# Kernel optimization log

Hardware: AMD Instinct MI355X
Metric: run time of the kernel (lower is better)

Reference implementation:

```python
import jax, jax.numpy as jnp
import numpy as np

N_NODES = 170000
N_EDGES = 1200000
IN_FEATS = 128
N_HIDDEN = 256
N_CLASSES = 40
BN_EPS = 1e-5


def setup_inputs() -> dict:
    key = jax.random.key(0)
    ks = jax.random.split(key, 12)
    feat = jax.random.normal(ks[0], (N_NODES, IN_FEATS), dtype=jnp.float32)
    src = jax.random.randint(ks[1], (N_EDGES,), 0, N_NODES, dtype=jnp.int32)
    dst = jax.random.randint(ks[2], (N_EDGES,), 0, N_NODES, dtype=jnp.int32)
    # GraphConv weights (glorot-ish scale) and last-layer bias
    W0 = jax.random.normal(ks[3], (IN_FEATS, N_HIDDEN), dtype=jnp.float32) * (1.0 / np.sqrt(IN_FEATS))
    W1 = jax.random.normal(ks[4], (N_HIDDEN, N_HIDDEN), dtype=jnp.float32) * (1.0 / np.sqrt(N_HIDDEN))
    W2 = jax.random.normal(ks[5], (N_HIDDEN, N_CLASSES), dtype=jnp.float32) * (1.0 / np.sqrt(N_HIDDEN))
    b2 = jnp.zeros((N_CLASSES,), dtype=jnp.float32)
    # BatchNorm affine params for the two hidden layers
    g0 = jnp.ones((N_HIDDEN,), dtype=jnp.float32)
    beta0 = jnp.zeros((N_HIDDEN,), dtype=jnp.float32)
    g1 = jnp.ones((N_HIDDEN,), dtype=jnp.float32)
    beta1 = jnp.zeros((N_HIDDEN,), dtype=jnp.float32)
    return {"feat": feat, "src": src, "dst": dst, "W0": W0, "W1": W1, "W2": W2,
            "b2": b2, "g0": g0, "beta0": beta0, "g1": g1, "beta1": beta1}


def _batchnorm(h, gamma, beta):
    mean = jnp.mean(h, axis=0)
    var = jnp.mean((h - mean) ** 2, axis=0)  # biased var, torch training-mode norm
    return (h - mean) * jax.lax.rsqrt(var + BN_EPS) * gamma + beta


def reference(feat, src, dst, W0, W1, W2, b2, g0, beta0, g1, beta1):
    n = feat.shape[0]
    ones_e = jnp.ones(src.shape, dtype=feat.dtype)
    deg_out = jnp.clip(jax.ops.segment_sum(ones_e, src, num_segments=n), 1.0)
    deg_in = jnp.clip(jax.ops.segment_sum(ones_e, dst, num_segments=n), 1.0)
    norm_src = deg_out ** -0.5  # [N]
    norm_dst = deg_in ** -0.5   # [N]

    def conv(h, W, bias=None):
        # GraphConv 'both': D_out^{-1/2} message, sum-aggregate, D_in^{-1/2}
        h = h @ W                              # project first (out <= in)
        msg = h[src] * norm_src[src][:, None]  # [E, out]
        agg = jax.ops.segment_sum(msg, dst, num_segments=n) * norm_dst[:, None]
        if bias is not None:
            agg = agg + bias
        return agg

    # dropout layers are identity in this deterministic (eval-style) reference
    h = conv(feat, W0)
    h = jax.nn.relu(_batchnorm(h, g0, beta0))
    h = conv(h, W1)
    h = jax.nn.relu(_batchnorm(h, g1, beta1))
    h = conv(h, W2, b2)
    return h
```

## Files before the change

### kernel.cpp

```cpp
#include <hip/hip_runtime.h>

#define NN 170000
#define NE 1200000
#define F_IN 128
#define F_HID 256
#define F_OUT 40
#define BN_EPS 1e-5f
#define SCAN_B ((NN + 255) / 256)

typedef __attribute__((ext_vector_type(8))) short short8;
typedef __attribute__((ext_vector_type(4))) float f32x4;
typedef __attribute__((ext_vector_type(4))) unsigned short us4;

__device__ __forceinline__ float b2f(unsigned short u) {
    union { unsigned x; float f; } c; c.x = ((unsigned)u) << 16; return c.f;
}
__device__ __forceinline__ unsigned short f2b(float f) {
    union { float f; unsigned x; } c; c.f = f;
    unsigned r = (c.x + 0x7FFFu + ((c.x >> 16) & 1u)) >> 16;
    return (unsigned short)r;
}
__device__ __forceinline__ unsigned bn2(unsigned u, float a0, float b0, float a1, float b1) {
    float lo = b2f((unsigned short)(u & 0xffffu));
    float hi = b2f((unsigned short)(u >> 16));
    lo = fmaxf(lo * a0 + b0, 0.0f);
    hi = fmaxf(hi * a1 + b1, 0.0f);
    return (unsigned)f2b(lo) | ((unsigned)f2b(hi) << 16);
}

__global__ void count_kernel(const int* __restrict__ src, const int* __restrict__ dst,
                             int* __restrict__ cnt_src, int* __restrict__ cnt_dst, int E) {
    int e = blockIdx.x * blockDim.x + threadIdx.x;
    if (e < E) {
        atomicAdd(&cnt_src[src[e]], 1);
        atomicAdd(&cnt_dst[dst[e]], 1);
    }
}

__global__ void norm_kernel(const int* __restrict__ cnt_src, const int* __restrict__ cnt_dst,
                            float* __restrict__ norm_src, float* __restrict__ norm_dst, int N) {
    int i = blockIdx.x * blockDim.x + threadIdx.x;
    if (i < N) {
        norm_src[i] = rsqrtf((float)max(cnt_src[i], 1));
        norm_dst[i] = rsqrtf((float)max(cnt_dst[i], 1));
    }
}

__global__ void scan_block_kernel(const int* __restrict__ cnt, int* __restrict__ local,
                                  int* __restrict__ partials, int N) {
    __shared__ int s[256];
    int t = threadIdx.x;
    int idx = blockIdx.x * 256 + t;
    int v = (idx < N) ? cnt[idx] : 0;
    s[t] = v;
    __syncthreads();
    #pragma unroll
    for (int off = 1; off < 256; off <<= 1) {
        int x = (t >= off) ? s[t - off] : 0;
        __syncthreads();
        s[t] += x;
        __syncthreads();
    }
    if (idx < N) local[idx] = s[t] - v;
    if (t == 255) partials[blockIdx.x] = s[t];
}

__global__ void scan_partials_kernel(int* __restrict__ partials, int B) {
    __shared__ int s[1024];
    int t = threadIdx.x;
    int v = (t < B) ? partials[t] : 0;
    s[t] = v;
    __syncthreads();
    #pragma unroll
    for (int off = 1; off < 1024; off <<= 1) {
        int x = (t >= off) ? s[t - off] : 0;
        __syncthreads();
        s[t] += x;
        __syncthreads();
    }
    if (t < B) partials[t] = s[t] - v;
}

__global__ void scan_add_kernel(const int* __restrict__ local, const int* __restrict__ partials,
                                int* __restrict__ row_ptr, int N) {
    int idx = blockIdx.x * blockDim.x + threadIdx.x;
    if (idx < N) row_ptr[idx] = local[idx] + partials[idx >> 8];
    if (idx == 0) row_ptr[N] = NE;
}

__global__ void fill_kernel(const int* __restrict__ src, const int* __restrict__ dst,
                            const int* __restrict__ row_ptr, int* __restrict__ fill,
                            int* __restrict__ csr_src, int E) {
    int e = blockIdx.x * blockDim.x + threadIdx.x;
    if (e < E) {
        int d = dst[e];
        int pos = row_ptr[d] + atomicAdd(&fill[d], 1);
        csr_src[pos] = src[e];
    }
}

__global__ void cast_feat_kernel(const float* __restrict__ feat, unsigned short* __restrict__ featb) {
    unsigned idx = blockIdx.x * blockDim.x + threadIdx.x;
    if (idx >= (unsigned)NN * (F_IN / 4)) return;
    const float* p = feat + (size_t)idx * 4;
    f32x4 v = __builtin_nontemporal_load((const f32x4*)p);
    us4 o; o.x = f2b(v.x); o.y = f2b(v.y); o.z = f2b(v.z); o.w = f2b(v.w);
    *(us4*)(featb + (size_t)idx * 4) = o;
}

__global__ void gather0_kernel(const unsigned short* __restrict__ h, const int* __restrict__ row_ptr,
                               const int* __restrict__ csr_src, const float* __restrict__ norm_src,
                               unsigned short* __restrict__ out, int N) {
    constexpr int TPN = F_IN / 4;
    unsigned idx = blockIdx.x * blockDim.x + threadIdx.x;
    if (idx >= (unsigned)N * TPN) return;
    unsigned node = idx / TPN;
    unsigned g = idx % TPN;
    int beg = row_ptr[node], end = row_ptr[node + 1];
    float ax = 0.f, ay = 0.f, az = 0.f, aw = 0.f;
    for (int e = beg; e < end; e++) {
        int s = csr_src[e];
        float ns = norm_src[s];
        const us4 v = *(const us4*)(h + (size_t)s * F_IN + g * 4);
        ax += b2f(v.x) * ns; ay += b2f(v.y) * ns; az += b2f(v.z) * ns; aw += b2f(v.w) * ns;
    }
    us4 o; o.x = f2b(ax); o.y = f2b(ay); o.z = f2b(az); o.w = f2b(aw);
    __builtin_nontemporal_store(o, (us4*)(out + (size_t)node * F_IN + g * 4));
}

__global__ void gather1_bn_kernel(const unsigned short* __restrict__ h, const int* __restrict__ row_ptr,
                                  const int* __restrict__ csr_src, const float* __restrict__ norm_src,
                                  const float* __restrict__ bna, const float* __restrict__ bnb,
                                  unsigned short* __restrict__ out, int N) {
    constexpr int TPN = F_HID / 4;
    unsigned idx = blockIdx.x * blockDim.x + threadIdx.x;
    if (idx >= (unsigned)N * TPN) return;
    unsigned node = idx / TPN;
    unsigned g = idx % TPN;
    const f32x4 a4 = *(const f32x4*)(bna + g * 4);
    const f32x4 b4 = *(const f32x4*)(bnb + g * 4);
    int beg = row_ptr[node], end = row_ptr[node + 1];
    float ax = 0.f, ay = 0.f, az = 0.f, aw = 0.f;
    for (int e = beg; e < end; e++) {
        int s = csr_src[e];
        float ns = norm_src[s];
        const us4 v = *(const us4*)(h + (size_t)s * F_HID + g * 4);
        ax += fmaxf(b2f(v.x) * a4.x + b4.x, 0.f) * ns;
        ay += fmaxf(b2f(v.y) * a4.y + b4.y, 0.f) * ns;
        az += fmaxf(b2f(v.z) * a4.z + b4.z, 0.f) * ns;
        aw += fmaxf(b2f(v.w) * a4.w + b4.w, 0.f) * ns;
    }
    us4 o; o.x = f2b(ax); o.y = f2b(ay); o.z = f2b(az); o.w = f2b(aw);
    __builtin_nontemporal_store(o, (us4*)(out + (size_t)node * F_HID + g * 4));
}

__global__ void gather_final_kernel(const float* __restrict__ h, const int* __restrict__ row_ptr,
                                    const int* __restrict__ csr_src, const float* __restrict__ norm_src,
                                    const float* __restrict__ norm_dst, const float* __restrict__ bias,
                                    float* __restrict__ out, int N) {
    constexpr int TPN = F_OUT / 4;
    unsigned idx = blockIdx.x * blockDim.x + threadIdx.x;
    if (idx >= (unsigned)N * TPN) return;
    unsigned node = idx / TPN;
    unsigned g = idx % TPN;
    int beg = row_ptr[node], end = row_ptr[node + 1];
    float ax = 0.f, ay = 0.f, az = 0.f, aw = 0.f;
    for (int e = beg; e < end; e++) {
        int s = csr_src[e];
        float ns = norm_src[s];
        const f32x4 v = *(const f32x4*)(h + (size_t)s * F_OUT + g * 4);
        ax += v.x * ns; ay += v.y * ns; az += v.z * ns; aw += v.w * ns;
    }
    float nd = norm_dst[node];
    const f32x4 b = *(const f32x4*)(bias + g * 4);
    f32x4 r;
    r.x = ax * nd + b.x; r.y = ay * nd + b.y; r.z = az * nd + b.z; r.w = aw * nd + b.w;
    __builtin_nontemporal_store(r, (f32x4*)(out + (size_t)node * F_OUT + g * 4));
}

template<int K, int M, int MP>
__global__ void wt_kernel(const float* __restrict__ W, unsigned short* __restrict__ Wt) {
    int idx = blockIdx.x * blockDim.x + threadIdx.x;
    if (idx >= MP * K) return;
    int m = idx / K, k = idx % K;
    float v = (m < M) ? W[(size_t)k * M + m] : 0.0f;
    Wt[idx] = f2b(v);
}

__global__ void bn_finalize_kernel(const float* __restrict__ sum, const float* __restrict__ sumsq,
                                   const float* __restrict__ gamma, const float* __restrict__ beta,
                                   float* __restrict__ a, float* __restrict__ b) {
    int c = threadIdx.x;
    float invN = 1.0f / (float)NN;
    float mean = sum[c] * invN;
    float var = sumsq[c] * invN - mean * mean;
    float inv = rsqrtf(var + BN_EPS);
    float ac = inv * gamma[c];
    a[c] = ac;
    b[c] = beta[c] - mean * ac;
}

template<int K, int BN_T, int WM_T, int WN_T, int WAVES_N, bool SCALE, bool BF16OUT, int M_OUT,
         bool STATS, bool APPLYBN>
__global__ __launch_bounds__(256) void mfma_gemm(const unsigned short* __restrict__ A,
                                                 const unsigned short* __restrict__ Wt,
                                                 const float* __restrict__ norm_dst,
                                                 void* __restrict__ C,
                                                 const float* __restrict__ bna,
                                                 const float* __restrict__ bnb,
                                                 float* __restrict__ osum,
                                                 float* __restrict__ osumsq, int N) {
    constexpr int BM = 128, BK = 64, AP = 72;
    __shared__ unsigned short As[BM * AP];
    __shared__ unsigned short Bs[BN_T * AP];

    const int lane = threadIdx.x & 63;
    const int wave = threadIdx.x >> 6;
    const int wr = wave / WAVES_N, wc = wave % WAVES_N;
    const int quad = lane >> 4, l15 = lane & 15;
    const int r0 = blockIdx.y * BM;
    const int c0 = blockIdx.x * BN_T;
    const int wmb = wr * WM_T * 16;
    const int wnb = wc * WN_T * 16;

    f32x4 acc[WM_T][WN_T] = {};

    for (int k0 = 0; k0 < K; k0 += BK) {
        #pragma unroll
        for (int p = 0; p < BM * (BK / 8) / 256; p++) {
            int c = threadIdx.x + p * 256;
            int row = c >> 3, off = (c & 7) * 8;
            int gr = r0 + row;
            uint4 v = make_uint4(0, 0, 0, 0);
            if (gr < N) {
                v = *(const uint4*)(A + (size_t)gr * K + k0 + off);
                if (APPLYBN) {
                    int kb = k0 + off;
                    const f32x4 a0 = *(const f32x4*)(bna + kb);
                    const f32x4 a1 = *(const f32x4*)(bna + kb + 4);
                    const f32x4 s0 = *(const f32x4*)(bnb + kb);
                    const f32x4 s1 = *(const f32x4*)(bnb + kb + 4);
                    v.x = bn2(v.x, a0.x, s0.x, a0.y, s0.y);
                    v.y = bn2(v.y, a0.z, s0.z, a0.w, s0.w);
                    v.z = bn2(v.z, a1.x, s1.x, a1.y, s1.y);
                    v.w = bn2(v.w, a1.z, s1.z, a1.w, s1.w);
                }
            }
            *(uint4*)(As + row * AP + off) = v;
        }
        #pragma unroll
        for (int p = 0; p < BN_T * (BK / 8) / 256; p++) {
            int c = threadIdx.x + p * 256;
            int m = c >> 3, off = (c & 7) * 8;
            *(uint4*)(Bs + m * AP + off) = *(const uint4*)(Wt + (size_t)(c0 + m) * K + k0 + off);
        }
        __syncthreads();
        #pragma unroll
        for (int kk = 0; kk < BK; kk += 32) {
            short8 af[WM_T], bf[WN_T];
            #pragma unroll
            for (int i = 0; i < WM_T; i++)
                af[i] = *(const short8*)(As + (wmb + i * 16 + l15) * AP + kk + quad * 8);
            #pragma unroll
            for (int j = 0; j < WN_T; j++)
                bf[j] = *(const short8*)(Bs + (wnb + j * 16 + l15) * AP + kk + quad * 8);
            #pragma unroll
            for (int i = 0; i < WM_T; i++)
                #pragma unroll
                for (int j = 0; j < WN_T; j++)
                    acc[i][j] = __builtin_amdgcn_mfma_f32_16x16x32_bf16(af[i], bf[j], acc[i][j], 0, 0, 0);
        }
        __syncthreads();
    }

    float s[WN_T] = {}, ss[WN_T] = {};
    #pragma unroll
    for (int i = 0; i < WM_T; i++) {
        #pragma unroll
        for (int r = 0; r < 4; r++) {
            int row = r0 + wmb + i * 16 + quad * 4 + r;
            if (row >= N) continue;
            float scale = SCALE ? norm_dst[row] : 1.0f;
            #pragma unroll
            for (int j = 0; j < WN_T; j++) {
                float v = acc[i][j][r] * scale;
                if (STATS) { s[j] += v; ss[j] += v * v; }
                int col = c0 + wnb + j * 16 + l15;
                if (col < M_OUT) {
                    if (BF16OUT) ((unsigned short*)C)[(size_t)row * M_OUT + col] = f2b(v);
                    else         ((float*)C)[(size_t)row * M_OUT + col] = v;
                }
            }
        }
    }
    if (STATS) {
        #pragma unroll
        for (int j = 0; j < WN_T; j++) {
            float t = s[j], t2 = ss[j];
            t  += __shfl_xor(t, 16);  t  += __shfl_xor(t, 32);
            t2 += __shfl_xor(t2, 16); t2 += __shfl_xor(t2, 32);
            if (quad == 0) {
                int col = c0 + wnb + j * 16 + l15;
                atomicAdd(&osum[col], t);
                atomicAdd(&osumsq[col], t2);
            }
        }
    }
}

extern "C" void kernel_launch(void* const* d_in, const int* in_sizes, int n_in,
                              void* d_out, int out_size, void* d_ws, size_t ws_size,
                              hipStream_t stream) {
    const float* feat  = (const float*)d_in[0];
    const int*   src   = (const int*)d_in[1];
    const int*   dst   = (const int*)d_in[2];
    const float* W0    = (const float*)d_in[3];
    const float* W1    = (const float*)d_in[4];
    const float* W2    = (const float*)d_in[5];
    const float* b2    = (const float*)d_in[6];
    const float* g0    = (const float*)d_in[7];
    const float* beta0 = (const float*)d_in[8];
    const float* g1    = (const float*)d_in[9];
    const float* beta1 = (const float*)d_in[10];
    float* out = (float*)d_out;

    const int N = NN, E = NE;

    char* ws = (char*)d_ws;
    auto alloc_b = [&](size_t bytes) {
        void* p = (void*)ws;
        ws += ((bytes + 255) / 256) * 256;
        return p;
    };
    float* norm_src = (float*)alloc_b((size_t)N * 4);
    float* norm_dst = (float*)alloc_b((size_t)N * 4);
    int*   row_ptr  = (int*)alloc_b((size_t)(N + 1) * 4);
    int*   csr_src  = (int*)alloc_b((size_t)E * 4);
    float* bnsum    = (float*)alloc_b(512 * 4);
    float* bn_a0    = (float*)alloc_b(256 * 4);
    float* bn_b0    = (float*)alloc_b(256 * 4);
    float* bn_a1    = (float*)alloc_b(256 * 4);
    float* bn_b1    = (float*)alloc_b(256 * 4);
    unsigned short* Wt0 = (unsigned short*)alloc_b((size_t)256 * 128 * 2);
    unsigned short* Wt1 = (unsigned short*)alloc_b((size_t)256 * 256 * 2);
    unsigned short* Wt2 = (unsigned short*)alloc_b((size_t)64 * 256 * 2);
    void* B1 = alloc_b((size_t)N * 512);
    void* B2 = alloc_b((size_t)N * 512);
    unsigned short* featb = (unsigned short*)alloc_b((size_t)N * F_IN * 2);
    float* bnsumsq = bnsum + 256;

    unsigned short* B1b = (unsigned short*)B1;
    unsigned short* B2b = (unsigned short*)B2;
    float*          B1f = (float*)B1;

    int* cnt_src  = (int*)B1;
    int* cnt_dst  = cnt_src + N;
    int* fill     = cnt_dst + N;
    int* local    = fill + N;
    int* partials = local + N;

    hipMemsetAsync(cnt_src, 0, ((size_t)4 * N + 1024) * 4, stream);
    count_kernel<<<(E + 255) / 256, 256, 0, stream>>>(src, dst, cnt_src, cnt_dst, E);
    norm_kernel<<<(N + 255) / 256, 256, 0, stream>>>(cnt_src, cnt_dst, norm_src, norm_dst, N);
    scan_block_kernel<<<SCAN_B, 256, 0, stream>>>(cnt_dst, local, partials, N);
    scan_partials_kernel<<<1, 1024, 0, stream>>>(partials, SCAN_B);
    scan_add_kernel<<<(N + 255) / 256, 256, 0, stream>>>(local, partials, row_ptr, N);
    fill_kernel<<<(E + 255) / 256, 256, 0, stream>>>(src, dst, row_ptr, fill, csr_src, E);
    wt_kernel<128, 256, 256><<<(256 * 128 + 255) / 256, 256, 0, stream>>>(W0, Wt0);
    wt_kernel<256, 256, 256><<<(256 * 256 + 255) / 256, 256, 0, stream>>>(W1, Wt1);
    wt_kernel<256, 40, 64><<<(64 * 256 + 255) / 256, 256, 0, stream>>>(W2, Wt2);
    cast_feat_kernel<<<((unsigned)N * (F_IN / 4) + 255) / 256, 256, 0, stream>>>(feat, featb);

    const int GB = (N + 127) / 128;

    {
        unsigned total = (unsigned)N * (F_IN / 4);
        gather0_kernel<<<(total + 255) / 256, 256, 0, stream>>>(featb, row_ptr, csr_src, norm_src, B1b, N);
    }
    hipMemsetAsync(bnsum, 0, 512 * 4, stream);
    mfma_gemm<128, 128, 4, 4, 2, true, true, 256, true, false><<<dim3(2, GB), 256, 0, stream>>>(
        B1b, Wt0, norm_dst, B2, nullptr, nullptr, bnsum, bnsumsq, N);
    bn_finalize_kernel<<<1, 256, 0, stream>>>(bnsum, bnsumsq, g0, beta0, bn_a0, bn_b0);

    {
        unsigned total = (unsigned)N * (F_HID / 4);
        gather1_bn_kernel<<<(total + 255) / 256, 256, 0, stream>>>(
            B2b, row_ptr, csr_src, norm_src, bn_a0, bn_b0, B1b, N);
    }
    hipMemsetAsync(bnsum, 0, 512 * 4, stream);
    mfma_gemm<256, 128, 4, 4, 2, true, true, 256, true, false><<<dim3(2, GB), 256, 0, stream>>>(
        B1b, Wt1, norm_dst, B2, nullptr, nullptr, bnsum, bnsumsq, N);
    bn_finalize_kernel<<<1, 256, 0, stream>>>(bnsum, bnsumsq, g1, beta1, bn_a1, bn_b1);

    mfma_gemm<256, 64, 2, 4, 1, false, false, 40, false, true><<<dim3(1, GB), 256, 0, stream>>>(
        B2b, Wt2, nullptr, B1, bn_a1, bn_b1, nullptr, nullptr, N);
    {
        unsigned total = (unsigned)N * (F_OUT / 4);
        gather_final_kernel<<<(total + 255) / 256, 256, 0, stream>>>(
            B1f, row_ptr, csr_src, norm_src, norm_dst, b2, out, N);
    }
}
```

Baseline: 881.3 us.

## Prescale by source norm before gathers and widen GEMM tiles to full width

Folds the per-source degree normalization into the producer side: into the feature cast, into a new BN+ReLU+scale pass before the second gather, and into the final GEMM epilogue. The gathers then become pure sums with no random norm_src lookups, and the loops are unrolled by two with split accumulators. The hidden-layer GEMMs switch to a single 256-wide column tile per block so A is loaded once instead of twice. In exchange it adds an extra elementwise pass over the 256-wide hidden buffer and raises register pressure in the GEMM.

```diff
diff --git a/kernel.cpp b/kernel.cpp
--- a/kernel.cpp
+++ b/kernel.cpp
@@ -11,6 +11,7 @@
 typedef __attribute__((ext_vector_type(8))) short short8;
 typedef __attribute__((ext_vector_type(4))) float f32x4;
 typedef __attribute__((ext_vector_type(4))) unsigned short us4;
+typedef __attribute__((ext_vector_type(4))) unsigned int u32x4;
 
 __device__ __forceinline__ float b2f(unsigned short u) {
     union { unsigned x; float f; } c; c.x = ((unsigned)u) << 16; return c.f;
@@ -99,63 +100,69 @@
     }
 }
 
-__global__ void cast_feat_kernel(const float* __restrict__ feat, unsigned short* __restrict__ featb) {
+__global__ void cast_feat_kernel(const float* __restrict__ feat, const float* __restrict__ norm_src,
+                                 unsigned short* __restrict__ featb) {
     unsigned idx = blockIdx.x * blockDim.x + threadIdx.x;
     if (idx >= (unsigned)NN * (F_IN / 4)) return;
-    const float* p = feat + (size_t)idx * 4;
-    f32x4 v = __builtin_nontemporal_load((const f32x4*)p);
-    us4 o; o.x = f2b(v.x); o.y = f2b(v.y); o.z = f2b(v.z); o.w = f2b(v.w);
+    float ns = norm_src[idx / (F_IN / 4)];
+    f32x4 v = __builtin_nontemporal_load((const f32x4*)(feat + (size_t)idx * 4));
+    us4 o; o.x = f2b(v.x * ns); o.y = f2b(v.y * ns); o.z = f2b(v.z * ns); o.w = f2b(v.w * ns);
     *(us4*)(featb + (size_t)idx * 4) = o;
 }
 
-__global__ void gather0_kernel(const unsigned short* __restrict__ h, const int* __restrict__ row_ptr,
-                               const int* __restrict__ csr_src, const float* __restrict__ norm_src,
-                               unsigned short* __restrict__ out, int N) {
-    constexpr int TPN = F_IN / 4;
+__global__ void apply_bn_scale_kernel(const unsigned short* __restrict__ in,
+                                      const float* __restrict__ bna, const float* __restrict__ bnb,
+                                      const float* __restrict__ norm_src,
+                                      unsigned short* __restrict__ outp) {
+    unsigned idx = blockIdx.x * blockDim.x + threadIdx.x;
+    if (idx >= (unsigned)NN * (F_HID / 8)) return;
+    unsigned row = idx / (F_HID / 8);
+    unsigned c8 = (idx % (F_HID / 8)) * 8;
+    float ns = norm_src[row];
+    u32x4 u = *(const u32x4*)(in + (size_t)idx * 8);
+    const f32x4 a0 = *(const f32x4*)(bna + c8);
+    const f32x4 a1 = *(const f32x4*)(bna + c8 + 4);
+    const f32x4 s0 = *(const f32x4*)(bnb + c8);
+    const f32x4 s1 = *(const f32x4*)(bnb + c8 + 4);
+    u.x = bn2(u.x, a0.x * ns, s0.x * ns, a0.y * ns, s0.y * ns);
+    u.y = bn2(u.y, a0.z * ns, s0.z * ns, a0.w * ns, s0.w * ns);
+    u.z = bn2(u.z, a1.x * ns, s1.x * ns, a1.y * ns, s1.y * ns);
+    u.w = bn2(u.w, a1.z * ns, s1.z * ns, a1.w * ns, s1.w * ns);
+    __builtin_nontemporal_store(u, (u32x4*)(outp + (size_t)idx * 8));
+}
+
+template<int F>
+__global__ void gather_sum_kernel(const unsigned short* __restrict__ h, const int* __restrict__ row_ptr,
+                                  const int* __restrict__ csr_src,
+                                  unsigned short* __restrict__ out, int N) {
+    constexpr int TPN = F / 4;
     unsigned idx = blockIdx.x * blockDim.x + threadIdx.x;
     if (idx >= (unsigned)N * TPN) return;
     unsigned node = idx / TPN;
     unsigned g = idx % TPN;
     int beg = row_ptr[node], end = row_ptr[node + 1];
-    float ax = 0.f, ay = 0.f, az = 0.f, aw = 0.f;
-    for (int e = beg; e < end; e++) {
-        int s = csr_src[e];
-        float ns = norm_src[s];
-        const us4 v = *(const us4*)(h + (size_t)s * F_IN + g * 4);
-        ax += b2f(v.x) * ns; ay += b2f(v.y) * ns; az += b2f(v.z) * ns; aw += b2f(v.w) * ns;
-    }
-    us4 o; o.x = f2b(ax); o.y = f2b(ay); o.z = f2b(az); o.w = f2b(aw);
-    __builtin_nontemporal_store(o, (us4*)(out + (size_t)node * F_IN + g * 4));
-}
-
-__global__ void gather1_bn_kernel(const unsigned short* __restrict__ h, const int* __restrict__ row_ptr,
-                                  const int* __restrict__ csr_src, const float* __restrict__ norm_src,
-                                  const float* __restrict__ bna, const float* __restrict__ bnb,
-                                  unsigned short* __restrict__ out, int N) {
-    constexpr int TPN = F_HID / 4;
-    unsigned idx = blockIdx.x * blockDim.x + threadIdx.x;
-    if (idx >= (unsigned)N * TPN) return;
-    unsigned node = idx / TPN;
-    unsigned g = idx % TPN;
-    const f32x4 a4 = *(const f32x4*)(bna + g * 4);
-    const f32x4 b4 = *(const f32x4*)(bnb + g * 4);
-    int beg = row_ptr[node], end = row_ptr[node + 1];
-    float ax = 0.f, ay = 0.f, az = 0.f, aw = 0.f;
-    for (int e = beg; e < end; e++) {
-        int s = csr_src[e];
-        float ns = norm_src[s];
-        const us4 v = *(const us4*)(h + (size_t)s * F_HID + g * 4);
-        ax += fmaxf(b2f(v.x) * a4.x + b4.x, 0.f) * ns;
-        ay += fmaxf(b2f(v.y) * a4.y + b4.y, 0.f) * ns;
-        az += fmaxf(b2f(v.z) * a4.z + b4.z, 0.f) * ns;
-        aw += fmaxf(b2f(v.w) * a4.w + b4.w, 0.f) * ns;
-    }
-    us4 o; o.x = f2b(ax); o.y = f2b(ay); o.z = f2b(az); o.w = f2b(aw);
-    __builtin_nontemporal_store(o, (us4*)(out + (size_t)node * F_HID + g * 4));
+    float ax0 = 0.f, ay0 = 0.f, az0 = 0.f, aw0 = 0.f;
+    float ax1 = 0.f, ay1 = 0.f, az1 = 0.f, aw1 = 0.f;
+    int e = beg;
+    for (; e + 2 <= end; e += 2) {
+        int s0 = csr_src[e], s1 = csr_src[e + 1];
+        const us4 v0 = *(const us4*)(h + (size_t)s0 * F + g * 4);
+        const us4 v1 = *(const us4*)(h + (size_t)s1 * F + g * 4);
+        ax0 += b2f(v0.x); ay0 += b2f(v0.y); az0 += b2f(v0.z); aw0 += b2f(v0.w);
+        ax1 += b2f(v1.x); ay1 += b2f(v1.y); az1 += b2f(v1.z); aw1 += b2f(v1.w);
+    }
+    if (e < end) {
+        int s0 = csr_src[e];
+        const us4 v0 = *(const us4*)(h + (size_t)s0 * F + g * 4);
+        ax0 += b2f(v0.x); ay0 += b2f(v0.y); az0 += b2f(v0.z); aw0 += b2f(v0.w);
+    }
+    us4 o;
+    o.x = f2b(ax0 + ax1); o.y = f2b(ay0 + ay1); o.z = f2b(az0 + az1); o.w = f2b(aw0 + aw1);
+    __builtin_nontemporal_store(o, (us4*)(out + (size_t)node * F + g * 4));
 }
 
 __global__ void gather_final_kernel(const float* __restrict__ h, const int* __restrict__ row_ptr,
-                                    const int* __restrict__ csr_src, const float* __restrict__ norm_src,
+                                    const int* __restrict__ csr_src,
                                     const float* __restrict__ norm_dst, const float* __restrict__ bias,
                                     float* __restrict__ out, int N) {
     constexpr int TPN = F_OUT / 4;
@@ -164,17 +171,26 @@
     unsigned node = idx / TPN;
     unsigned g = idx % TPN;
     int beg = row_ptr[node], end = row_ptr[node + 1];
-    float ax = 0.f, ay = 0.f, az = 0.f, aw = 0.f;
-    for (int e = beg; e < end; e++) {
-        int s = csr_src[e];
-        float ns = norm_src[s];
-        const f32x4 v = *(const f32x4*)(h + (size_t)s * F_OUT + g * 4);
-        ax += v.x * ns; ay += v.y * ns; az += v.z * ns; aw += v.w * ns;
+    float ax0 = 0.f, ay0 = 0.f, az0 = 0.f, aw0 = 0.f;
+    float ax1 = 0.f, ay1 = 0.f, az1 = 0.f, aw1 = 0.f;
+    int e = beg;
+    for (; e + 2 <= end; e += 2) {
+        int s0 = csr_src[e], s1 = csr_src[e + 1];
+        const f32x4 v0 = *(const f32x4*)(h + (size_t)s0 * F_OUT + g * 4);
+        const f32x4 v1 = *(const f32x4*)(h + (size_t)s1 * F_OUT + g * 4);
+        ax0 += v0.x; ay0 += v0.y; az0 += v0.z; aw0 += v0.w;
+        ax1 += v1.x; ay1 += v1.y; az1 += v1.z; aw1 += v1.w;
+    }
+    if (e < end) {
+        int s0 = csr_src[e];
+        const f32x4 v0 = *(const f32x4*)(h + (size_t)s0 * F_OUT + g * 4);
+        ax0 += v0.x; ay0 += v0.y; az0 += v0.z; aw0 += v0.w;
     }
     float nd = norm_dst[node];
     const f32x4 b = *(const f32x4*)(bias + g * 4);
     f32x4 r;
-    r.x = ax * nd + b.x; r.y = ay * nd + b.y; r.z = az * nd + b.z; r.w = aw * nd + b.w;
+    r.x = (ax0 + ax1) * nd + b.x; r.y = (ay0 + ay1) * nd + b.y;
+    r.z = (az0 + az1) * nd + b.z; r.w = (aw0 + aw1) * nd + b.w;
     __builtin_nontemporal_store(r, (f32x4*)(out + (size_t)node * F_OUT + g * 4));
 }
 
@@ -204,7 +220,7 @@
          bool STATS, bool APPLYBN>
 __global__ __launch_bounds__(256) void mfma_gemm(const unsigned short* __restrict__ A,
                                                  const unsigned short* __restrict__ Wt,
-                                                 const float* __restrict__ norm_dst,
+                                                 const float* __restrict__ rowscale,
                                                  void* __restrict__ C,
                                                  const float* __restrict__ bna,
                                                  const float* __restrict__ bnb,
@@ -231,9 +247,9 @@
             int c = threadIdx.x + p * 256;
             int row = c >> 3, off = (c & 7) * 8;
             int gr = r0 + row;
-            uint4 v = make_uint4(0, 0, 0, 0);
+            u32x4 v = {0u, 0u, 0u, 0u};
             if (gr < N) {
-                v = *(const uint4*)(A + (size_t)gr * K + k0 + off);
+                v = *(const u32x4*)(A + (size_t)gr * K + k0 + off);
                 if (APPLYBN) {
                     int kb = k0 + off;
                     const f32x4 a0 = *(const f32x4*)(bna + kb);
@@ -246,13 +262,13 @@
                     v.w = bn2(v.w, a1.z, s1.z, a1.w, s1.w);
                 }
             }
-            *(uint4*)(As + row * AP + off) = v;
+            *(u32x4*)(As + row * AP + off) = v;
         }
         #pragma unroll
         for (int p = 0; p < BN_T * (BK / 8) / 256; p++) {
             int c = threadIdx.x + p * 256;
             int m = c >> 3, off = (c & 7) * 8;
-            *(uint4*)(Bs + m * AP + off) = *(const uint4*)(Wt + (size_t)(c0 + m) * K + k0 + off);
+            *(u32x4*)(Bs + m * AP + off) = *(const u32x4*)(Wt + (size_t)(c0 + m) * K + k0 + off);
         }
         __syncthreads();
         #pragma unroll
@@ -280,7 +296,7 @@
         for (int r = 0; r < 4; r++) {
             int row = r0 + wmb + i * 16 + quad * 4 + r;
             if (row >= N) continue;
-            float scale = SCALE ? norm_dst[row] : 1.0f;
+            float scale = SCALE ? rowscale[row] : 1.0f;
             #pragma unroll
             for (int j = 0; j < WN_T; j++) {
                 float v = acc[i][j][r] * scale;
@@ -351,7 +367,7 @@
 
     unsigned short* B1b = (unsigned short*)B1;
     unsigned short* B2b = (unsigned short*)B2;
-    float*          B1f = (float*)B1;
+    float*          B2f = (float*)B2;
 
     int* cnt_src  = (int*)B1;
     int* cnt_dst  = cnt_src + N;
@@ -369,34 +385,35 @@
     wt_kernel<128, 256, 256><<<(256 * 128 + 255) / 256, 256, 0, stream>>>(W0, Wt0);
     wt_kernel<256, 256, 256><<<(256 * 256 + 255) / 256, 256, 0, stream>>>(W1, Wt1);
     wt_kernel<256, 40, 64><<<(64 * 256 + 255) / 256, 256, 0, stream>>>(W2, Wt2);
-    cast_feat_kernel<<<((unsigned)N * (F_IN / 4) + 255) / 256, 256, 0, stream>>>(feat, featb);
+    cast_feat_kernel<<<((unsigned)N * (F_IN / 4) + 255) / 256, 256, 0, stream>>>(feat, norm_src, featb);
 
     const int GB = (N + 127) / 128;
 
     {
         unsigned total = (unsigned)N * (F_IN / 4);
-        gather0_kernel<<<(total + 255) / 256, 256, 0, stream>>>(featb, row_ptr, csr_src, norm_src, B1b, N);
+        gather_sum_kernel<F_IN><<<(total + 255) / 256, 256, 0, stream>>>(featb, row_ptr, csr_src, B1b, N);
     }
     hipMemsetAsync(bnsum, 0, 512 * 4, stream);
-    mfma_gemm<128, 128, 4, 4, 2, true, true, 256, true, false><<<dim3(2, GB), 256, 0, stream>>>(
+    mfma_gemm<128, 256, 4, 8, 2, true, true, 256, true, false><<<dim3(1, GB), 256, 0, stream>>>(
         B1b, Wt0, norm_dst, B2, nullptr, nullptr, bnsum, bnsumsq, N);
     bn_finalize_kernel<<<1, 256, 0, stream>>>(bnsum, bnsumsq, g0, beta0, bn_a0, bn_b0);
 
+    apply_bn_scale_kernel<<<((unsigned)N * (F_HID / 8) + 255) / 256, 256, 0, stream>>>(
+        B2b, bn_a0, bn_b0, norm_src, B1b);
     {
         unsigned total = (unsigned)N * (F_HID / 4);
-        gather1_bn_kernel<<<(total + 255) / 256, 256, 0, stream>>>(
-            B2b, row_ptr, csr_src, norm_src, bn_a0, bn_b0, B1b, N);
+        gather_sum_kernel<F_HID><<<(total + 255) / 256, 256, 0, stream>>>(B1b, row_ptr, csr_src, B2b, N);
     }
     hipMemsetAsync(bnsum, 0, 512 * 4, stream);
-    mfma_gemm<256, 128, 4, 4, 2, true, true, 256, true, false><<<dim3(2, GB), 256, 0, stream>>>(
-        B1b, Wt1, norm_dst, B2, nullptr, nullptr, bnsum, bnsumsq, N);
+    mfma_gemm<256, 256, 4, 8, 2, true, true, 256, true, false><<<dim3(1, GB), 256, 0, stream>>>(
+        B2b, Wt1, norm_dst, B1, nullptr, nullptr, bnsum, bnsumsq, N);
     bn_finalize_kernel<<<1, 256, 0, stream>>>(bnsum, bnsumsq, g1, beta1, bn_a1, bn_b1);
 
-    mfma_gemm<256, 64, 2, 4, 1, false, false, 40, false, true><<<dim3(1, GB), 256, 0, stream>>>(
-        B2b, Wt2, nullptr, B1, bn_a1, bn_b1, nullptr, nullptr, N);
+    mfma_gemm<256, 64, 2, 4, 1, true, false, 40, false, true><<<dim3(1, GB), 256, 0, stream>>>(
+        B1b, Wt2, norm_src, B2, bn_a1, bn_b1, nullptr, nullptr, N);
     {
         unsigned total = (unsigned)N * (F_OUT / 4);
         gather_final_kernel<<<(total + 255) / 256, 256, 0, stream>>>(
-            B1f, row_ptr, csr_src, norm_src, norm_dst, b2, out, N);
-    }
-}
+            B2f, row_ptr, csr_src, norm_dst, b2, out, N);
+    }
+}
```

After: 937.3 us. 1.06x slower.
